# Kernel tuning notes

Measured on AMD Instinct MI355X. Metric: run time of the kernel, lower is better.

## Reference

```python
import jax, jax.numpy as jnp
import numpy as np

M_FIELDS = 26   # cin_size[0]
H1 = 128        # cin_size[1]
H2 = 128        # cin_size[2]
BATCH = 2048
EMB_K = 32


def setup_inputs() -> dict:
    key = jax.random.key(0)
    k0, k1, k2, k3, k4 = jax.random.split(key, 5)
    inputs = jax.random.normal(k0, (BATCH, M_FIELDS, EMB_K), dtype=jnp.float32)
    # Conv3d(1, H1, kernel=(26,26,1)) -> weight [H1, H_prev=26, m=26], bias [H1]
    W1 = jax.random.normal(k1, (H1, M_FIELDS, M_FIELDS), dtype=jnp.float32) * 0.05
    b1 = jax.random.normal(k2, (H1,), dtype=jnp.float32) * 0.05
    # Conv3d(1, H2, kernel=(H1,26,1)) -> weight [H2, H1, m=26], bias [H2]
    W2 = jax.random.normal(k3, (H2, H1, M_FIELDS), dtype=jnp.float32) * 0.05
    b2 = jax.random.normal(k4, (H2,), dtype=jnp.float32) * 0.05
    return {"inputs": inputs, "W1": W1, "b1": b1, "W2": W2, "b2": b2}


def _cin_layer(x_prev, x0, W, b):
    # x_prev: [B, H_prev, k], x0: [B, m, k], W: [H, H_prev, m], b: [H]
    # Equivalent to: outer product z[b,i,j,k] = x_prev[b,i,k]*x0[b,j,k],
    # then Conv3d with kernel (H_prev, m, 1): out[b,h,k] = sum_ij W[h,i,j]*z + b[h]
    return jnp.einsum('bik,bjk,hij->bhk', x_prev, x0, W) + b[None, :, None]


def reference(inputs, W1, b1, W2, b2):
    x1 = _cin_layer(inputs, inputs, W1, b1)   # [B, H1, k]
    x2 = _cin_layer(x1, inputs, W2, b2)       # [B, H2, k]
    res = jnp.concatenate([x1, x2], axis=1)   # [B, H1+H2, k]
    return jnp.sum(res, axis=-1)              # [B, H1+H2]
```

## Files before the change

### kernel.cpp

```cpp
#include <hip/hip_runtime.h>

typedef __bf16 bf16;
typedef __bf16 bf16x8 __attribute__((ext_vector_type(8)));
typedef __bf16 bf16x4 __attribute__((ext_vector_type(4)));
typedef float f32x4 __attribute__((ext_vector_type(4)));
typedef unsigned int u32;

#define NB    2048
#define NM    26
#define NJP   27

__device__ __forceinline__ bf16x8 splat8(u32 p) {
  union { u32 u[4]; bf16x8 v; } s;
  s.u[0] = p; s.u[1] = p; s.u[2] = p; s.u[3] = p;
  return s.v;
}

__device__ __forceinline__ u32 dup16(float v) {
  union { bf16 h; unsigned short s; } cv; cv.h = (bf16)v;
  return (u32)cv.s * 0x10001u;
}

__global__ __launch_bounds__(256) void prep_all(
    const float* __restrict__ W1, const float* __restrict__ W2,
    bf16* __restrict__ w1t, bf16* __restrict__ w2t2)
{
  const int bid = blockIdx.x, t = threadIdx.x;
  #pragma unroll
  for (int g = 0; g < 4; ++g) {
    int ge = g*160768 + bid*256 + t;
    if (ge < 110592) {
      int e = ge;
      int el = e & 7, lr = (e >> 3) & 15, lq = (e >> 7) & 3, ni = (e >> 9) & 3;
      int rest = e >> 11;
      int c = rest % NJP, cs_idx = rest / NJP;
      int h = cs_idx*64 + ni*16 + lr;
      int i = lq*8 + el;
      float v = (i < NM && c < NM) ? W1[h*(NM*NM) + i*NM + c] : 0.f;
      w1t[e] = (bf16)v;
    } else {
      int e = ge - 110592;
      int el = e & 7, lr = (e >> 3) & 15, lq = (e >> 7) & 3, ni = (e >> 9) & 3;
      int rest = e >> 11;
      int kc = rest % 130, cs_idx = rest / 130;
      int h = cs_idx*64 + ni*16 + lr;
      int c = lq*8 + el;
      float v = (kc < 128 && c < NM) ? W2[h*(128*NM) + kc*NM + c] : 0.f;
      w2t2[e] = (bf16)v;
    }
  }
}

#define STEP(CUR, NXT, J) do {                                                 \
  { int jn = ((J)+1 > 25) ? 25 : (J)+1;         \
    sc[NXT][0] = dup16(spw[jn*32]);                                            \
    sc[NXT][1] = dup16(spw[jn*32 + 16]); }                                     \
  _Pragma("unroll")                                                            \
  for (int ni = 0; ni < 4; ++ni)                                               \
    B[NXT][ni] = *(const bf16x8*)(tb + (long)((J)+1)*2048 + ni*512);           \
  _Pragma("unroll")                                                            \
  for (int mi = 0; mi < 2; ++mi) {                                             \
    bf16x8 af = xf[mi] * splat8(sc[CUR][mi]);                                  \
    _Pragma("unroll")                                                          \
    for (int ni = 0; ni < 4; ++ni)                                             \
      acc[mi][ni] = __builtin_amdgcn_mfma_f32_16x16x32_bf16(af, B[CUR][ni],    \
                                                            acc[mi][ni], 0, 0, 0); \
  }                                                                            \
} while (0)

__global__ __launch_bounds__(256, 4) void cin1G(
    const float* __restrict__ in, const bf16* __restrict__ w1t,
    const float* __restrict__ b1, bf16* __restrict__ G2, float* __restrict__ out)
{
  __shared__ __align__(16) bf16 ldsT[4][64*36];
  const int t = threadIdx.x;
  const int bid = blockIdx.x;
  const int lane = t & 63, w = t >> 6;
  const int x = bid & 7, u = bid >> 3;
  const int m8 = (u >> 4)*8 + x;
  const int v = u & 15;
  const int strip = m8*8 + (v >> 1);
  const int cs_idx = v & 1, cs = cs_idx * 64;
  const int lr = lane & 15, lq = lane >> 4;
  const int fo = lq*128 + lr*8;
  const int bw = strip*4 + w;

  const float* bin = in + (long)bw*(NM*32);
  const float* spw = bin + lr;

  bf16x8 xf[2];
  #pragma unroll
  for (int mi = 0; mi < 2; ++mi)
    #pragma unroll
    for (int e = 0; e < 8; ++e) {
      int j = lq*8 + e;
      xf[mi][e] = (bf16)((j < NM) ? bin[j*32 + mi*16 + lr] : 0.f);
    }

  f32x4 acc[2][4];
  #pragma unroll
  for (int mi=0; mi<2; ++mi)
    #pragma unroll
    for (int ni=0; ni<4; ++ni) acc[mi][ni] = {0.f,0.f,0.f,0.f};

  const bf16* tb = w1t + (long)cs_idx*NJP*2048 + fo;

  u32 sc[2][2];
  bf16x8 B[2][4];
  #pragma unroll
  for (int ni = 0; ni < 4; ++ni)
    B[0][ni] = *(const bf16x8*)(tb + ni*512);
  sc[0][0] = dup16(spw[0]);  sc[0][1] = dup16(spw[16]);

  for (int jj = 0; jj < 13; ++jj) {
    STEP(0, 1, 2*jj);
    STEP(1, 0, 2*jj + 1);
  }

  float bias[4];
  #pragma unroll
  for (int ni=0; ni<4; ++ni) bias[ni] = b1[cs + ni*16 + lr];

  #pragma unroll
  for (int ni=0; ni<4; ++ni) {
    float vv = 0.f;
    #pragma unroll
    for (int mi=0; mi<2; ++mi)
      #pragma unroll
      for (int r=0; r<4; ++r) vv += acc[mi][ni][r];
    vv += __shfl_xor(vv, 16, 64);
    vv += __shfl_xor(vv, 32, 64);
    if (lq == 0) out[bw*256 + cs + ni*16 + lr] = vv + 32.0f * bias[ni];
  }

  bf16* T = &ldsT[w][0];
  #pragma unroll
  for (int mi=0; mi<2; ++mi)
    #pragma unroll
    for (int ni=0; ni<4; ++ni) {
      bf16x4 pk;
      #pragma unroll
      for (int r=0; r<4; ++r) pk[r] = (bf16)(acc[mi][ni][r] + bias[ni]);
      *(bf16x4*)&T[(ni*16+lr)*36 + mi*16 + lq*4] = pk;
    }

  bf16x8 bg[2];
  #pragma unroll
  for (int nt = 0; nt < 2; ++nt) {
    int j = nt*16 + lr;
    bf16x8 vv;
    #pragma unroll
    for (int e=0; e<8; ++e) vv[e] = (bf16)0.f;
    if (j < NM) {
      const float* src = bin + j*32 + lq*8;
      f32x4 a = *(const f32x4*)src, c = *(const f32x4*)(src+4);
      #pragma unroll
      for (int e=0; e<4; ++e) { vv[e] = (bf16)a[e]; vv[4+e] = (bf16)c[e]; }
    }
    bg[nt] = vv;
  }
  const long gbase = (long)(bw >> 5)*131072 + (bw & 31)*8;
  #pragma unroll
  for (int mt = 0; mt < 4; ++mt) {
    bf16x8 ag = *(const bf16x8*)&T[(mt*16+lr)*36 + lq*8];
    #pragma unroll
    for (int nt = 0; nt < 2; ++nt) {
      f32x4 z = {0.f,0.f,0.f,0.f};
      f32x4 g = __builtin_amdgcn_mfma_f32_16x16x32_bf16(bg[nt], ag, z, 0, 0, 0);
      bf16x4 pk;
      #pragma unroll
      for (int r = 0; r < 4; ++r) pk[r] = (bf16)g[r];
      const int kh = (cs + mt*16 + lr)*4 + nt*2 + (lq >> 1);
      *(bf16x4*)&G2[gbase + (long)kh*256 + (lq & 1)*4] = pk;
    }
  }
}

#define STEPG(CUR, NXT, KN) do {                                               \
  _Pragma("unroll")                                                            \
  for (int mi = 0; mi < 2; ++mi)                                               \
    A[NXT][mi] = *(const bf16x8*)(Ab + (long)(KN)*1024 + mi*128);              \
  _Pragma("unroll")                                                            \
  for (int ni = 0; ni < 4; ++ni)                                               \
    B[NXT][ni] = *(const bf16x8*)(tbc + (long)(KN)*2048 + ni*512);             \
  _Pragma("unroll")                                                            \
  for (int mi = 0; mi < 2; ++mi)                                               \
    _Pragma("unroll")                                                          \
    for (int ni = 0; ni < 4; ++ni)                                             \
      acc[mi][ni] = __builtin_amdgcn_mfma_f32_16x16x32_bf16(A[CUR][mi],        \
                                  B[CUR][ni], acc[mi][ni], 0, 0, 0);           \
} while (0)

__global__ __launch_bounds__(256, 4) void gemm2(
    const bf16* __restrict__ G2, const bf16* __restrict__ w2t2,
    const float* __restrict__ b2, float* __restrict__ out)
{
  const int t = threadIdx.x;
  const int lane = t & 63, w = t >> 6;
  const int s = blockIdx.x >> 5;
  const int q32 = blockIdx.x & 31;
  const int x = q32 & 7, q = q32 >> 3;
  const int ms = x + q*16 + (w >> 1)*8;
  const int cs_idx = w & 1;
  const int lr = lane & 15, lq = lane >> 4;
  const int fo = lq*128 + lr*8;
  const int kc0 = s*8;

  const bf16* Ab  = G2 + ((long)(ms*512 + lq)*32 + lr)*8;
  const bf16* tbc = w2t2 + (long)cs_idx*130*2048 + fo;

  f32x4 acc[2][4];
  #pragma unroll
  for (int mi=0; mi<2; ++mi)
    #pragma unroll
    for (int ni=0; ni<4; ++ni) acc[mi][ni] = {0.f,0.f,0.f,0.f};

  bf16x8 A[2][2], B[2][4];
  #pragma unroll
  for (int mi=0; mi<2; ++mi)
    A[0][mi] = *(const bf16x8*)(Ab + (long)kc0*1024 + mi*128);
  #pragma unroll
  for (int ni=0; ni<4; ++ni)
    B[0][ni] = *(const bf16x8*)(tbc + (long)kc0*2048 + ni*512);

  for (int jj = 0; jj < 4; ++jj) {
    STEPG(0, 1, kc0 + 2*jj + 1);
    STEPG(1, 0, kc0 + 2*jj + 2);
  }

  if (s == 0) {
    #pragma unroll
    for (int ni=0; ni<4; ++ni) {
      float bv = 32.0f * b2[cs_idx*64 + ni*16 + lr];
      #pragma unroll
      for (int mi=0; mi<2; ++mi)
        #pragma unroll
        for (int r=0; r<4; ++r) acc[mi][ni][r] += bv;
    }
  }

  #pragma unroll
  for (int mi=0; mi<2; ++mi)
    #pragma unroll
    for (int ni=0; ni<4; ++ni) {
      int h = cs_idx*64 + ni*16 + lr;
      #pragma unroll
      for (int r=0; r<4; ++r) {
        int b = ms*32 + mi*16 + lq*4 + r;
        atomicAdd(&out[b*256 + 128 + h], acc[mi][ni][r]);
      }
    }
}

extern "C" void kernel_launch(void* const* d_in, const int* in_sizes, int n_in,
                              void* d_out, int out_size, void* d_ws, size_t ws_size,
                              hipStream_t stream) {
  const float* in = (const float*)d_in[0];
  const float* W1 = (const float*)d_in[1];
  const float* b1 = (const float*)d_in[2];
  const float* W2 = (const float*)d_in[3];
  const float* b2 = (const float*)d_in[4];
  float* out = (float*)d_out;

  char* ws = (char*)d_ws;
  bf16* w1t  = (bf16*)(ws);
  bf16* w2t2 = (bf16*)(ws + 1048576);
  bf16* G2   = (bf16*)(ws + 4194304);

  prep_all<<<628,  256, 0, stream>>>(W1, W2, w1t, w2t2);
  cin1G   <<<1024, 256, 0, stream>>>(in, w1t, b1, G2, out);
  gemm2   <<<512,  256, 0, stream>>>(G2, w2t2, b2, out);
}
```

Before: 112.8 us.

## Drop weight prep kernel; stage bf16 weight tiles into LDS inside each kernel

Removes the separate prep_all launch that converted W1/W2 into swizzled bf16 global buffers. Each cin1G and gemm2 block now reads its slice of the fp32 weights, converts it and lays it out in shared memory, then streams MFMA B-operands from LDS instead of global memory. cin1G is split into finer 32-column h tiles with twice as many blocks, and occupancy hints are lowered to 2 blocks per SIMD group. This saves one launch and a global round trip, but every block redoes the fp32 weight conversion with scalar strided loads, and the larger LDS footprint can limit how many blocks fit.

```diff
diff --git a/kernel.cpp b/kernel.cpp
--- a/kernel.cpp
+++ b/kernel.cpp
@@ -6,9 +6,7 @@
 typedef float f32x4 __attribute__((ext_vector_type(4)));
 typedef unsigned int u32;
 
-#define NB    2048
-#define NM    26
-#define NJP   27
+#define NM 26
 
 __device__ __forceinline__ bf16x8 splat8(u32 p) {
   union { u32 u[4]; bf16x8 v; } s;
@@ -21,69 +19,55 @@
   return (u32)cv.s * 0x10001u;
 }
 
-__global__ __launch_bounds__(256) void prep_all(
-    const float* __restrict__ W1, const float* __restrict__ W2,
-    bf16* __restrict__ w1t, bf16* __restrict__ w2t2)
-{
-  const int bid = blockIdx.x, t = threadIdx.x;
-  #pragma unroll
-  for (int g = 0; g < 4; ++g) {
-    int ge = g*160768 + bid*256 + t;
-    if (ge < 110592) {
-      int e = ge;
-      int el = e & 7, lr = (e >> 3) & 15, lq = (e >> 7) & 3, ni = (e >> 9) & 3;
-      int rest = e >> 11;
-      int c = rest % NJP, cs_idx = rest / NJP;
-      int h = cs_idx*64 + ni*16 + lr;
-      int i = lq*8 + el;
-      float v = (i < NM && c < NM) ? W1[h*(NM*NM) + i*NM + c] : 0.f;
-      w1t[e] = (bf16)v;
-    } else {
-      int e = ge - 110592;
-      int el = e & 7, lr = (e >> 3) & 15, lq = (e >> 7) & 3, ni = (e >> 9) & 3;
-      int rest = e >> 11;
-      int kc = rest % 130, cs_idx = rest / 130;
-      int h = cs_idx*64 + ni*16 + lr;
-      int c = lq*8 + el;
-      float v = (kc < 128 && c < NM) ? W2[h*(128*NM) + kc*NM + c] : 0.f;
-      w2t2[e] = (bf16)v;
-    }
-  }
-}
-
 #define STEP(CUR, NXT, J) do {                                                 \
-  { int jn = ((J)+1 > 25) ? 25 : (J)+1;         \
+  { int jn = ((J)+1 > 25) ? 25 : (J)+1;                                        \
     sc[NXT][0] = dup16(spw[jn*32]);                                            \
     sc[NXT][1] = dup16(spw[jn*32 + 16]); }                                     \
   _Pragma("unroll")                                                            \
-  for (int ni = 0; ni < 4; ++ni)                                               \
-    B[NXT][ni] = *(const bf16x8*)(tb + (long)((J)+1)*2048 + ni*512);           \
+  for (int ni = 0; ni < 2; ++ni)                                               \
+    Bf[NXT][ni] = *(const bf16x8*)&ldsB[((J)+1)*1024 + ni*512 + fo];           \
   _Pragma("unroll")                                                            \
   for (int mi = 0; mi < 2; ++mi) {                                             \
     bf16x8 af = xf[mi] * splat8(sc[CUR][mi]);                                  \
     _Pragma("unroll")                                                          \
-    for (int ni = 0; ni < 4; ++ni)                                             \
-      acc[mi][ni] = __builtin_amdgcn_mfma_f32_16x16x32_bf16(af, B[CUR][ni],    \
+    for (int ni = 0; ni < 2; ++ni)                                             \
+      acc[mi][ni] = __builtin_amdgcn_mfma_f32_16x16x32_bf16(af, Bf[CUR][ni],   \
                                                             acc[mi][ni], 0, 0, 0); \
   }                                                                            \
 } while (0)
 
-__global__ __launch_bounds__(256, 4) void cin1G(
-    const float* __restrict__ in, const bf16* __restrict__ w1t,
+__global__ __launch_bounds__(256, 2) void cin1G(
+    const float* __restrict__ in, const float* __restrict__ W1,
     const float* __restrict__ b1, bf16* __restrict__ G2, float* __restrict__ out)
 {
-  __shared__ __align__(16) bf16 ldsT[4][64*36];
-  const int t = threadIdx.x;
-  const int bid = blockIdx.x;
+  __shared__ __align__(16) bf16 ldsB[27*1024];
+  __shared__ __align__(16) bf16 ldsT[4][32*36];
+  const int t = threadIdx.x, bid = blockIdx.x;
   const int lane = t & 63, w = t >> 6;
-  const int x = bid & 7, u = bid >> 3;
-  const int m8 = (u >> 4)*8 + x;
-  const int v = u & 15;
-  const int strip = m8*8 + (v >> 1);
-  const int cs_idx = v & 1, cs = cs_idx * 64;
   const int lr = lane & 15, lq = lane >> 4;
   const int fo = lq*128 + lr*8;
-  const int bw = strip*4 + w;
+  const int x = bid & 7, mid = (bid >> 3) & 31, hi = bid >> 8;
+  const int ms = hi*8 + x, sub = mid >> 2, qq = mid & 3;
+  const int h0 = qq*32;
+  const int bw = (ms*8 + sub)*4 + w;
+
+  #pragma unroll
+  for (int r = 0; r < 4; ++r) {
+    int task = r*256 + t;
+    int hl = task >> 5, i = task & 31;
+    const float* srcr = W1 + (h0 + hl)*(NM*NM) + i*NM;
+    int dstb = (hl >> 4)*512 + (i >> 3)*128 + (hl & 15)*8 + (i & 7);
+    if (i < NM) {
+      #pragma unroll
+      for (int c = 0; c < NM; ++c) ldsB[c*1024 + dstb] = (bf16)srcr[c];
+    } else {
+      #pragma unroll
+      for (int c = 0; c < NM; ++c) ldsB[c*1024 + dstb] = (bf16)0.f;
+    }
+  }
+  { bf16x4 z4; z4[0] = z4[1] = z4[2] = z4[3] = (bf16)0.f;
+    *(bf16x4*)&ldsB[26*1024 + t*4] = z4; }
+  __syncthreads();
 
   const float* bin = in + (long)bw*(NM*32);
   const float* spw = bin + lr;
@@ -97,19 +81,17 @@
       xf[mi][e] = (bf16)((j < NM) ? bin[j*32 + mi*16 + lr] : 0.f);
     }
 
-  f32x4 acc[2][4];
-  #pragma unroll
-  for (int mi=0; mi<2; ++mi)
-    #pragma unroll
-    for (int ni=0; ni<4; ++ni) acc[mi][ni] = {0.f,0.f,0.f,0.f};
-
-  const bf16* tb = w1t + (long)cs_idx*NJP*2048 + fo;
+  f32x4 acc[2][2];
+  #pragma unroll
+  for (int mi=0; mi<2; ++mi)
+    #pragma unroll
+    for (int ni=0; ni<2; ++ni) acc[mi][ni] = {0.f,0.f,0.f,0.f};
 
   u32 sc[2][2];
-  bf16x8 B[2][4];
-  #pragma unroll
-  for (int ni = 0; ni < 4; ++ni)
-    B[0][ni] = *(const bf16x8*)(tb + ni*512);
+  bf16x8 Bf[2][2];
+  #pragma unroll
+  for (int ni = 0; ni < 2; ++ni)
+    Bf[0][ni] = *(const bf16x8*)&ldsB[ni*512 + fo];
   sc[0][0] = dup16(spw[0]);  sc[0][1] = dup16(spw[16]);
 
   for (int jj = 0; jj < 13; ++jj) {
@@ -117,12 +99,12 @@
     STEP(1, 0, 2*jj + 1);
   }
 
-  float bias[4];
-  #pragma unroll
-  for (int ni=0; ni<4; ++ni) bias[ni] = b1[cs + ni*16 + lr];
-
-  #pragma unroll
-  for (int ni=0; ni<4; ++ni) {
+  float bias[2];
+  #pragma unroll
+  for (int ni=0; ni<2; ++ni) bias[ni] = b1[h0 + ni*16 + lr];
+
+  #pragma unroll
+  for (int ni=0; ni<2; ++ni) {
     float vv = 0.f;
     #pragma unroll
     for (int mi=0; mi<2; ++mi)
@@ -130,14 +112,14 @@
       for (int r=0; r<4; ++r) vv += acc[mi][ni][r];
     vv += __shfl_xor(vv, 16, 64);
     vv += __shfl_xor(vv, 32, 64);
-    if (lq == 0) out[bw*256 + cs + ni*16 + lr] = vv + 32.0f * bias[ni];
+    if (lq == 0) out[bw*256 + h0 + ni*16 + lr] = vv + 32.0f * bias[ni];
   }
 
   bf16* T = &ldsT[w][0];
   #pragma unroll
   for (int mi=0; mi<2; ++mi)
     #pragma unroll
-    for (int ni=0; ni<4; ++ni) {
+    for (int ni=0; ni<2; ++ni) {
       bf16x4 pk;
       #pragma unroll
       for (int r=0; r<4; ++r) pk[r] = (bf16)(acc[mi][ni][r] + bias[ni]);
@@ -161,7 +143,7 @@
   }
   const long gbase = (long)(bw >> 5)*131072 + (bw & 31)*8;
   #pragma unroll
-  for (int mt = 0; mt < 4; ++mt) {
+  for (int mt = 0; mt < 2; ++mt) {
     bf16x8 ag = *(const bf16x8*)&T[(mt*16+lr)*36 + lq*8];
     #pragma unroll
     for (int nt = 0; nt < 2; ++nt) {
@@ -170,44 +152,62 @@
       bf16x4 pk;
       #pragma unroll
       for (int r = 0; r < 4; ++r) pk[r] = (bf16)g[r];
-      const int kh = (cs + mt*16 + lr)*4 + nt*2 + (lq >> 1);
+      const int kh = (h0 + mt*16 + lr)*4 + nt*2 + (lq >> 1);
       *(bf16x4*)&G2[gbase + (long)kh*256 + (lq & 1)*4] = pk;
     }
   }
 }
 
-#define STEPG(CUR, NXT, KN) do {                                               \
+#define STEPG(CUR, NXT, KNR) do {                                              \
   _Pragma("unroll")                                                            \
   for (int mi = 0; mi < 2; ++mi)                                               \
-    A[NXT][mi] = *(const bf16x8*)(Ab + (long)(KN)*1024 + mi*128);              \
-  _Pragma("unroll")                                                            \
-  for (int ni = 0; ni < 4; ++ni)                                               \
-    B[NXT][ni] = *(const bf16x8*)(tbc + (long)(KN)*2048 + ni*512);             \
-  _Pragma("unroll")                                                            \
-  for (int mi = 0; mi < 2; ++mi)                                               \
+    A[NXT][mi] = *(const bf16x8*)(Ab + (long)(kc0 + (KNR) + 1)*1024 + mi*128); \
+  _Pragma("unroll")                                                            \
+  for (int ni = 0; ni < 4; ++ni) {                                             \
+    bf16x8 bfr = *(const bf16x8*)&ldsW[(KNR)*2048 + ni*512 + fo];              \
     _Pragma("unroll")                                                          \
-    for (int ni = 0; ni < 4; ++ni)                                             \
+    for (int mi = 0; mi < 2; ++mi)                                             \
       acc[mi][ni] = __builtin_amdgcn_mfma_f32_16x16x32_bf16(A[CUR][mi],        \
-                                  B[CUR][ni], acc[mi][ni], 0, 0, 0);           \
+                                  bfr, acc[mi][ni], 0, 0, 0);                  \
+  }                                                                            \
 } while (0)
 
-__global__ __launch_bounds__(256, 4) void gemm2(
-    const bf16* __restrict__ G2, const bf16* __restrict__ w2t2,
+__global__ __launch_bounds__(256, 2) void gemm2(
+    const bf16* __restrict__ G2, const float* __restrict__ W2,
     const float* __restrict__ b2, float* __restrict__ out)
 {
-  const int t = threadIdx.x;
+  __shared__ __align__(16) bf16 ldsW[8*2048];
+  const int t = threadIdx.x, bid = blockIdx.x;
   const int lane = t & 63, w = t >> 6;
-  const int s = blockIdx.x >> 5;
-  const int q32 = blockIdx.x & 31;
-  const int x = q32 & 7, q = q32 >> 3;
-  const int ms = x + q*16 + (w >> 1)*8;
-  const int cs_idx = w & 1;
   const int lr = lane & 15, lq = lane >> 4;
   const int fo = lq*128 + lr*8;
+  const int x = bid & 7, u = bid >> 3;
+  const int s = u >> 2, csx = (u >> 1) & 1, mhi = u & 1;
+  const int msgrp = mhi*8 + x;
+  const int ms = w*16 + msgrp;
   const int kc0 = s*8;
 
-  const bf16* Ab  = G2 + ((long)(ms*512 + lq)*32 + lr)*8;
-  const bf16* tbc = w2t2 + (long)cs_idx*130*2048 + fo;
+  #pragma unroll
+  for (int r = 0; r < 2; ++r) {
+    int task = r*256 + t;
+    int kcrel = task >> 6, hl = task & 63;
+    int h = csx*64 + hl, kc = kc0 + kcrel;
+    const float* src = W2 + ((long)h*128 + kc)*NM;
+    int dstb = kcrel*2048 + (hl >> 4)*512 + (hl & 15)*8;
+    #pragma unroll
+    for (int cq = 0; cq < 4; ++cq) {
+      bf16x8 pk;
+      #pragma unroll
+      for (int el = 0; el < 8; ++el) {
+        int c = cq*8 + el;
+        pk[el] = (c < NM) ? (bf16)src[c] : (bf16)0.f;
+      }
+      *(bf16x8*)&ldsW[dstb + cq*128] = pk;
+    }
+  }
+  __syncthreads();
+
+  const bf16* Ab = G2 + ((long)(ms*512 + lq)*32 + lr)*8;
 
   f32x4 acc[2][4];
   #pragma unroll
@@ -215,23 +215,20 @@
     #pragma unroll
     for (int ni=0; ni<4; ++ni) acc[mi][ni] = {0.f,0.f,0.f,0.f};
 
-  bf16x8 A[2][2], B[2][4];
+  bf16x8 A[2][2];
   #pragma unroll
   for (int mi=0; mi<2; ++mi)
     A[0][mi] = *(const bf16x8*)(Ab + (long)kc0*1024 + mi*128);
-  #pragma unroll
-  for (int ni=0; ni<4; ++ni)
-    B[0][ni] = *(const bf16x8*)(tbc + (long)kc0*2048 + ni*512);
 
   for (int jj = 0; jj < 4; ++jj) {
-    STEPG(0, 1, kc0 + 2*jj + 1);
-    STEPG(1, 0, kc0 + 2*jj + 2);
+    STEPG(0, 1, 2*jj);
+    STEPG(1, 0, 2*jj + 1);
   }
 
   if (s == 0) {
     #pragma unroll
     for (int ni=0; ni<4; ++ni) {
-      float bv = 32.0f * b2[cs_idx*64 + ni*16 + lr];
+      float bv = 32.0f * b2[csx*64 + ni*16 + lr];
       #pragma unroll
       for (int mi=0; mi<2; ++mi)
         #pragma unroll
@@ -243,7 +240,7 @@
   for (int mi=0; mi<2; ++mi)
     #pragma unroll
     for (int ni=0; ni<4; ++ni) {
-      int h = cs_idx*64 + ni*16 + lr;
+      int h = csx*64 + ni*16 + lr;
       #pragma unroll
       for (int r=0; r<4; ++r) {
         int b = ms*32 + mi*16 + lq*4 + r;
@@ -262,12 +259,8 @@
   const float* b2 = (const float*)d_in[4];
   float* out = (float*)d_out;
 
-  char* ws = (char*)d_ws;
-  bf16* w1t  = (bf16*)(ws);
-  bf16* w2t2 = (bf16*)(ws + 1048576);
-  bf16* G2   = (bf16*)(ws + 4194304);
-
-  prep_all<<<628,  256, 0, stream>>>(W1, W2, w1t, w2t2);
-  cin1G   <<<1024, 256, 0, stream>>>(in, w1t, b1, G2, out);
-  gemm2   <<<512,  256, 0, stream>>>(G2, w2t2, b2, out);
-}
+  bf16* G2 = (bf16*)((char*)d_ws + 4194304);
+
+  cin1G<<<2048, 256, 0, stream>>>(in, W1, b1, G2, out);
+  gemm2<<<512,  256, 0, stream>>>(G2, W2, b2, out);
+}
```

Result: slower. 131.9 us (+16.9%).

## Process two batch rows per wave in cin1G to reuse W1 tile loads

Applied to the files above, without the earlier changes.

Each wave of the first CIN kernel now handles two batch elements instead of one. The W1 B-fragments loaded per step are shared across both rows, which halves weight traffic per output, and the grid shrinks from 1024 to 512 blocks. The scaled A operand is now computed in fp32 and then rounded, instead of as a packed bf16 multiply. In exchange, register use roughly doubles for accumulators and inputs, and launch bounds drop to 2 blocks per SM, which may reduce latency hiding. The block-to-strip mapping is also simplified, so the earlier swizzle is gone.

```diff
diff --git a/kernel.cpp b/kernel.cpp
--- a/kernel.cpp
+++ b/kernel.cpp
@@ -9,17 +9,6 @@
 #define NB    2048
 #define NM    26
 #define NJP   27
-
-__device__ __forceinline__ bf16x8 splat8(u32 p) {
-  union { u32 u[4]; bf16x8 v; } s;
-  s.u[0] = p; s.u[1] = p; s.u[2] = p; s.u[3] = p;
-  return s.v;
-}
-
-__device__ __forceinline__ u32 dup16(float v) {
-  union { bf16 h; unsigned short s; } cv; cv.h = (bf16)v;
-  return (u32)cv.s * 0x10001u;
-}
 
 __global__ __launch_bounds__(256) void prep_all(
     const float* __restrict__ W1, const float* __restrict__ W2,
@@ -53,64 +42,74 @@
 
 #define STEP(CUR, NXT, J) do {                                                 \
   { int jn = ((J)+1 > 25) ? 25 : (J)+1;         \
-    sc[NXT][0] = dup16(spw[jn*32]);                                            \
-    sc[NXT][1] = dup16(spw[jn*32 + 16]); }                                     \
+    scf[NXT][0][0] = spw0[jn*32];  scf[NXT][0][1] = spw0[jn*32 + 16];          \
+    scf[NXT][1][0] = spw1[jn*32];  scf[NXT][1][1] = spw1[jn*32 + 16]; }        \
   _Pragma("unroll")                                                            \
   for (int ni = 0; ni < 4; ++ni)                                               \
     B[NXT][ni] = *(const bf16x8*)(tb + (long)((J)+1)*2048 + ni*512);           \
   _Pragma("unroll")                                                            \
-  for (int mi = 0; mi < 2; ++mi) {                                             \
-    bf16x8 af = xf[mi] * splat8(sc[CUR][mi]);                                  \
+  for (int bb = 0; bb < 2; ++bb)                                               \
     _Pragma("unroll")                                                          \
-    for (int ni = 0; ni < 4; ++ni)                                             \
-      acc[mi][ni] = __builtin_amdgcn_mfma_f32_16x16x32_bf16(af, B[CUR][ni],    \
-                                                            acc[mi][ni], 0, 0, 0); \
-  }                                                                            \
+    for (int mi = 0; mi < 2; ++mi) {                                           \
+      bf16x8 af;                                                               \
+      _Pragma("unroll")                                                        \
+      for (int e = 0; e < 8; ++e)                                              \
+        af[e] = (bf16)(xf32[bb][mi][e] * scf[CUR][bb][mi]);                    \
+      _Pragma("unroll")                                                        \
+      for (int ni = 0; ni < 4; ++ni)                                           \
+        acc[bb][mi][ni] = __builtin_amdgcn_mfma_f32_16x16x32_bf16(af,          \
+                                    B[CUR][ni], acc[bb][mi][ni], 0, 0, 0);     \
+    }                                                                          \
 } while (0)
 
-__global__ __launch_bounds__(256, 4) void cin1G(
+__global__ __launch_bounds__(256, 2) void cin1G(
     const float* __restrict__ in, const bf16* __restrict__ w1t,
     const float* __restrict__ b1, bf16* __restrict__ G2, float* __restrict__ out)
 {
   __shared__ __align__(16) bf16 ldsT[4][64*36];
-  const int t = threadIdx.x;
-  const int bid = blockIdx.x;
+  const int t = threadIdx.x, bid = blockIdx.x;
   const int lane = t & 63, w = t >> 6;
-  const int x = bid & 7, u = bid >> 3;
-  const int m8 = (u >> 4)*8 + x;
-  const int v = u & 15;
-  const int strip = m8*8 + (v >> 1);
-  const int cs_idx = v & 1, cs = cs_idx * 64;
   const int lr = lane & 15, lq = lane >> 4;
   const int fo = lq*128 + lr*8;
-  const int bw = strip*4 + w;
-
-  const float* bin = in + (long)bw*(NM*32);
-  const float* spw = bin + lr;
-
-  bf16x8 xf[2];
-  #pragma unroll
-  for (int mi = 0; mi < 2; ++mi)
-    #pragma unroll
-    for (int e = 0; e < 8; ++e) {
-      int j = lq*8 + e;
-      xf[mi][e] = (bf16)((j < NM) ? bin[j*32 + mi*16 + lr] : 0.f);
-    }
-
-  f32x4 acc[2][4];
-  #pragma unroll
-  for (int mi=0; mi<2; ++mi)
-    #pragma unroll
-    for (int ni=0; ni<4; ++ni) acc[mi][ni] = {0.f,0.f,0.f,0.f};
+  const int cs_idx = bid & 1, cs = cs_idx * 64;
+  const int strip8 = bid >> 1;
+  const int bw0 = strip8*8 + w*2;
+
+  const float* bin0 = in + (long)bw0*(NM*32);
+  const float* bin1 = bin0 + NM*32;
+  const float* spw0 = bin0 + lr;
+  const float* spw1 = bin1 + lr;
+
+  float xf32[2][2][8];
+  #pragma unroll
+  for (int bb = 0; bb < 2; ++bb) {
+    const float* bin = bb ? bin1 : bin0;
+    #pragma unroll
+    for (int mi = 0; mi < 2; ++mi)
+      #pragma unroll
+      for (int e = 0; e < 8; ++e) {
+        int j = lq*8 + e;
+        xf32[bb][mi][e] = (j < NM) ? bin[j*32 + mi*16 + lr] : 0.f;
+      }
+  }
+
+  f32x4 acc[2][2][4];
+  #pragma unroll
+  for (int bb=0; bb<2; ++bb)
+    #pragma unroll
+    for (int mi=0; mi<2; ++mi)
+      #pragma unroll
+      for (int ni=0; ni<4; ++ni) acc[bb][mi][ni] = {0.f,0.f,0.f,0.f};
 
   const bf16* tb = w1t + (long)cs_idx*NJP*2048 + fo;
 
-  u32 sc[2][2];
+  float scf[2][2][2];
   bf16x8 B[2][4];
   #pragma unroll
   for (int ni = 0; ni < 4; ++ni)
     B[0][ni] = *(const bf16x8*)(tb + ni*512);
-  sc[0][0] = dup16(spw[0]);  sc[0][1] = dup16(spw[16]);
+  scf[0][0][0] = spw0[0];  scf[0][0][1] = spw0[16];
+  scf[0][1][0] = spw1[0];  scf[0][1][1] = spw1[16];
 
   for (int jj = 0; jj < 13; ++jj) {
     STEP(0, 1, 2*jj);
@@ -121,57 +120,64 @@
   #pragma unroll
   for (int ni=0; ni<4; ++ni) bias[ni] = b1[cs + ni*16 + lr];
 
-  #pragma unroll
-  for (int ni=0; ni<4; ++ni) {
-    float vv = 0.f;
+  bf16* T = &ldsT[w][0];
+
+  #pragma unroll
+  for (int bb = 0; bb < 2; ++bb) {
+    const int bw = bw0 + bb;
+    const float* bin = bb ? bin1 : bin0;
+
+    #pragma unroll
+    for (int ni=0; ni<4; ++ni) {
+      float vv = 0.f;
+      #pragma unroll
+      for (int mi=0; mi<2; ++mi)
+        #pragma unroll
+        for (int r=0; r<4; ++r) vv += acc[bb][mi][ni][r];
+      vv += __shfl_xor(vv, 16, 64);
+      vv += __shfl_xor(vv, 32, 64);
+      if (lq == 0) out[bw*256 + cs + ni*16 + lr] = vv + 32.0f * bias[ni];
+    }
+
     #pragma unroll
     for (int mi=0; mi<2; ++mi)
       #pragma unroll
-      for (int r=0; r<4; ++r) vv += acc[mi][ni][r];
-    vv += __shfl_xor(vv, 16, 64);
-    vv += __shfl_xor(vv, 32, 64);
-    if (lq == 0) out[bw*256 + cs + ni*16 + lr] = vv + 32.0f * bias[ni];
-  }
-
-  bf16* T = &ldsT[w][0];
-  #pragma unroll
-  for (int mi=0; mi<2; ++mi)
-    #pragma unroll
-    for (int ni=0; ni<4; ++ni) {
-      bf16x4 pk;
-      #pragma unroll
-      for (int r=0; r<4; ++r) pk[r] = (bf16)(acc[mi][ni][r] + bias[ni]);
-      *(bf16x4*)&T[(ni*16+lr)*36 + mi*16 + lq*4] = pk;
-    }
-
-  bf16x8 bg[2];
-  #pragma unroll
-  for (int nt = 0; nt < 2; ++nt) {
-    int j = nt*16 + lr;
-    bf16x8 vv;
-    #pragma unroll
-    for (int e=0; e<8; ++e) vv[e] = (bf16)0.f;
-    if (j < NM) {
-      const float* src = bin + j*32 + lq*8;
-      f32x4 a = *(const f32x4*)src, c = *(const f32x4*)(src+4);
-      #pragma unroll
-      for (int e=0; e<4; ++e) { vv[e] = (bf16)a[e]; vv[4+e] = (bf16)c[e]; }
-    }
-    bg[nt] = vv;
-  }
-  const long gbase = (long)(bw >> 5)*131072 + (bw & 31)*8;
-  #pragma unroll
-  for (int mt = 0; mt < 4; ++mt) {
-    bf16x8 ag = *(const bf16x8*)&T[(mt*16+lr)*36 + lq*8];
+      for (int ni=0; ni<4; ++ni) {
+        bf16x4 pk;
+        #pragma unroll
+        for (int r=0; r<4; ++r) pk[r] = (bf16)(acc[bb][mi][ni][r] + bias[ni]);
+        *(bf16x4*)&T[(ni*16+lr)*36 + mi*16 + lq*4] = pk;
+      }
+
+    bf16x8 bg[2];
     #pragma unroll
     for (int nt = 0; nt < 2; ++nt) {
-      f32x4 z = {0.f,0.f,0.f,0.f};
-      f32x4 g = __builtin_amdgcn_mfma_f32_16x16x32_bf16(bg[nt], ag, z, 0, 0, 0);
-      bf16x4 pk;
-      #pragma unroll
-      for (int r = 0; r < 4; ++r) pk[r] = (bf16)g[r];
-      const int kh = (cs + mt*16 + lr)*4 + nt*2 + (lq >> 1);
-      *(bf16x4*)&G2[gbase + (long)kh*256 + (lq & 1)*4] = pk;
+      int j = nt*16 + lr;
+      bf16x8 vv;
+      #pragma unroll
+      for (int e=0; e<8; ++e) vv[e] = (bf16)0.f;
+      if (j < NM) {
+        const float* src = bin + j*32 + lq*8;
+        f32x4 a = *(const f32x4*)src, c = *(const f32x4*)(src+4);
+        #pragma unroll
+        for (int e=0; e<4; ++e) { vv[e] = (bf16)a[e]; vv[4+e] = (bf16)c[e]; }
+      }
+      bg[nt] = vv;
+    }
+    const long gbase = (long)(bw >> 5)*131072 + (bw & 31)*8;
+    #pragma unroll
+    for (int mt = 0; mt < 4; ++mt) {
+      bf16x8 ag = *(const bf16x8*)&T[(mt*16+lr)*36 + lq*8];
+      #pragma unroll
+      for (int nt = 0; nt < 2; ++nt) {
+        f32x4 z = {0.f,0.f,0.f,0.f};
+        f32x4 g = __builtin_amdgcn_mfma_f32_16x16x32_bf16(bg[nt], ag, z, 0, 0, 0);
+        bf16x4 pk;
+        #pragma unroll
+        for (int r = 0; r < 4; ++r) pk[r] = (bf16)g[r];
+        const int kh = (cs + mt*16 + lr)*4 + nt*2 + (lq >> 1);
+        *(bf16x4*)&G2[gbase + (long)kh*256 + (lq & 1)*4] = pk;
+      }
     }
   }
 }
@@ -267,7 +273,7 @@
   bf16* w2t2 = (bf16*)(ws + 1048576);
   bf16* G2   = (bf16*)(ws + 4194304);
 
-  prep_all<<<628,  256, 0, stream>>>(W1, W2, w1t, w2t2);
-  cin1G   <<<1024, 256, 0, stream>>>(in, w1t, b1, G2, out);
-  gemm2   <<<512,  256, 0, stream>>>(G2, w2t2, b2, out);
-}
+  prep_all<<<628, 256, 0, stream>>>(W1, W2, w1t, w2t2);
+  cin1G  <<<512, 256, 0, stream>>>(in, w1t, b1, G2, out);
+  gemm2  <<<512, 256, 0, stream>>>(G2, w2t2, b2, out);
+}
```

After: 111.4 us. Within noise of the previous version (-1.2%).
